# Kernel tuning notes

Measured on AMD Instinct MI355X. Metric: run time of the kernel, lower is better.

The kernel has to match this reference:

```python
import jax, jax.numpy as jnp
import numpy as np

N_NODES = 100000
N_EDGES = 600000
D = 128
EPS = 1e-12  # F.normalize default eps


def _l2_normalize(v, axis=1):
    n = jnp.linalg.norm(v, axis=axis, keepdims=True)
    return v / jnp.maximum(n, EPS)


def setup_inputs() -> dict:
    key = jax.random.key(0)
    k1, k2, k3, k4, k5 = jax.random.split(key, 5)
    x = jax.random.normal(k1, (N_NODES, D), dtype=jnp.float32)
    edge_index = jax.random.randint(k2, (2, N_EDGES), 0, N_NODES, dtype=jnp.int64)
    edge_weight = jax.random.uniform(k3, (N_EDGES,), dtype=jnp.float32)
    W = jax.random.normal(k4, (D, 2 * D), dtype=jnp.float32) / np.sqrt(2 * D)
    b = jax.random.normal(k5, (D,), dtype=jnp.float32) * 0.01
    return {"x": x, "edge_index": edge_index, "edge_weight": edge_weight, "W": W, "b": b}


def reference(x, edge_index, edge_weight, W, b):
    src, dst = edge_index[0], edge_index[1]
    # message: x_j * edge_weight; aggregate: scatter-add at destination nodes
    msgs = x[src] * edge_weight[:, None]                       # [E, D]
    grads = jax.ops.segment_sum(msgs, dst, num_segments=N_NODES)  # [N, D]
    norm_grads = _l2_normalize(grads, axis=1)
    out = jnp.concatenate((x, norm_grads), axis=1)             # [N, 2D]
    out = out @ W.T + b                                        # Linear(2D -> D)
    return _l2_normalize(out, axis=1)
```

## Files before the change

### kernel.cpp

```cpp
#include <hip/hip_runtime.h>
#include <stdint.h>

typedef __attribute__((ext_vector_type(8))) short short8;
typedef __attribute__((ext_vector_type(4))) float f32x4;

__device__ __forceinline__ uint32_t f2bf1(float f) {
  union { float f; uint32_t u; } c; c.f = f;
  return (c.u + 0x7FFFu + ((c.u >> 16) & 1u)) >> 16;
}
__device__ __forceinline__ uint32_t pack2bf(float lo, float hi) {
  return f2bf1(lo) | (f2bf1(hi) << 16);
}
__device__ __forceinline__ float bflo(uint32_t u) {
  union { uint32_t u; float f; } c; c.u = u << 16; return c.f;
}
__device__ __forceinline__ float bfhi(uint32_t u) {
  union { uint32_t u; float f; } c; c.u = u & 0xFFFF0000u; return c.f;
}

__global__ void __launch_bounds__(256) prep_kernel(
    const int* __restrict__ dst, uint32_t* __restrict__ deg,
    uint32_t* __restrict__ pos,
    const float* __restrict__ x, uint32_t* __restrict__ cat,
    const float* __restrict__ W, uint32_t* __restrict__ Wb,
    int E, int N, int cB, int xB) {
  int b = blockIdx.x;
  if (b < cB) {
    int e = b * 256 + threadIdx.x;
    if (e < E) pos[e] = atomicAdd(&deg[dst[e]], 1u);
  } else if (b < cB + xB) {
    int n = (b - cB) * 4 + (threadIdx.x >> 6);
    if (n >= N) return;
    int lane = threadIdx.x & 63;
    float2 xv = reinterpret_cast<const float2*>(x + (size_t)n * 128)[lane];
    cat[(size_t)n * 128 + lane] = pack2bf(xv.x, xv.y);
  } else {
    int i = (b - cB - xB) * 256 + threadIdx.x;
    if (i < 16384) {
      float2 wv = reinterpret_cast<const float2*>(W)[i];
      Wb[i] = pack2bf(wv.x, wv.y);
    }
  }
}

__global__ void __launch_bounds__(256) scan1_kernel(
    const uint32_t* __restrict__ deg, uint32_t* __restrict__ partial,
    uint32_t* __restrict__ bsum, int N) {
  __shared__ uint32_t sm[256];
  int t = threadIdx.x;
  int base = blockIdx.x * 1024 + t * 4;
  uint32_t d0 = 0, d1 = 0, d2 = 0, d3 = 0;
  if (base + 3 < N) {
    uint4 v = *reinterpret_cast<const uint4*>(deg + base);
    d0 = v.x; d1 = v.y; d2 = v.z; d3 = v.w;
  } else {
    if (base + 0 < N) d0 = deg[base + 0];
    if (base + 1 < N) d1 = deg[base + 1];
    if (base + 2 < N) d2 = deg[base + 2];
    if (base + 3 < N) d3 = deg[base + 3];
  }
  uint32_t s4 = d0 + d1 + d2 + d3;
  sm[t] = s4;
  uint32_t v = s4;
  __syncthreads();
  #pragma unroll
  for (int off = 1; off < 256; off <<= 1) {
    uint32_t u = (t >= off) ? sm[t - off] : 0u;
    __syncthreads();
    v += u;
    sm[t] = v;
    __syncthreads();
  }
  uint32_t ex = v - s4;
  if (base + 0 < N) partial[base + 0] = ex;
  if (base + 1 < N) partial[base + 1] = ex + d0;
  if (base + 2 < N) partial[base + 2] = ex + d0 + d1;
  if (base + 3 < N) partial[base + 3] = ex + d0 + d1 + d2;
  if (t == 255) bsum[blockIdx.x] = v;
}

__global__ void __launch_bounds__(1024) scan2_kernel(
    const uint32_t* __restrict__ bsum, uint32_t* __restrict__ boff, int nb) {
  __shared__ uint32_t sm[1024];
  int t = threadIdx.x;
  uint32_t s = (t < nb) ? bsum[t] : 0u;
  sm[t] = s;
  uint32_t v = s;
  __syncthreads();
  #pragma unroll
  for (int off = 1; off < 1024; off <<= 1) {
    uint32_t u = (t >= off) ? sm[t - off] : 0u;
    __syncthreads();
    v += u;
    sm[t] = v;
    __syncthreads();
  }
  if (t < nb) boff[t] = v - s;
}

__global__ void __launch_bounds__(256) fill_kernel(
    const int* __restrict__ src, const int* __restrict__ dst,
    const float* __restrict__ ew, const uint32_t* __restrict__ partial,
    const uint32_t* __restrict__ boff, const uint32_t* __restrict__ pos,
    uint2* __restrict__ pairs, int E) {
  int e = blockIdx.x * 256 + threadIdx.x;
  if (e < E) {
    int d = dst[e];
    union { float f; uint32_t u; } w; w.f = ew[e];
    pairs[partial[d] + boff[d >> 10] + pos[e]] = make_uint2((uint32_t)src[e], w.u);
  }
}

__global__ void __launch_bounds__(256) gather_kernel(
    const uint2* __restrict__ pairs, const uint32_t* __restrict__ partial,
    const uint32_t* __restrict__ boff, const uint32_t* __restrict__ deg,
    uint32_t* __restrict__ cat, int N) {
  int n = blockIdx.x * 4 + (threadIdx.x >> 6);
  if (n >= N) return;
  int lane = threadIdx.x & 63;
  int sg = lane >> 4;
  int sl = lane & 15;
  uint32_t base = partial[n] + boff[n >> 10];
  int dn = (int)deg[n];

  uint2 mp = (lane < dn) ? pairs[base + lane] : make_uint2(0u, 0u);

  float a[8] = {0.f, 0.f, 0.f, 0.f, 0.f, 0.f, 0.f, 0.f};
  int iters = (dn + 3) >> 2;
  for (int i = 0; i < iters; ++i) {
    int k = i * 4 + sg;
    uint32_t su = (uint32_t)__shfl((int)mp.x, k, 64);
    uint32_t wu = (uint32_t)__shfl((int)mp.y, k, 64);
    if (k < dn) {
      union { uint32_t u; float f; } w; w.u = wu;
      uint4 v = reinterpret_cast<const uint4*>(cat + (size_t)su * 128)[sl];
      a[0] += w.f * bflo(v.x); a[1] += w.f * bfhi(v.x);
      a[2] += w.f * bflo(v.y); a[3] += w.f * bfhi(v.y);
      a[4] += w.f * bflo(v.z); a[5] += w.f * bfhi(v.z);
      a[6] += w.f * bflo(v.w); a[7] += w.f * bfhi(v.w);
    }
  }
  for (int k = 64 + sg; k < dn; k += 4) {
    uint2 p = pairs[base + k];
    union { uint32_t u; float f; } w; w.u = p.y;
    uint4 v = reinterpret_cast<const uint4*>(cat + (size_t)p.x * 128)[sl];
    a[0] += w.f * bflo(v.x); a[1] += w.f * bfhi(v.x);
    a[2] += w.f * bflo(v.y); a[3] += w.f * bfhi(v.y);
    a[4] += w.f * bflo(v.z); a[5] += w.f * bfhi(v.z);
    a[6] += w.f * bflo(v.w); a[7] += w.f * bfhi(v.w);
  }

  #pragma unroll
  for (int j = 0; j < 8; ++j) {
    a[j] += __shfl_xor(a[j], 16, 64);
    a[j] += __shfl_xor(a[j], 32, 64);
  }
  float ss = 0.f;
  #pragma unroll
  for (int j = 0; j < 8; ++j) ss += a[j] * a[j];
  ss += __shfl_xor(ss, 1, 64);
  ss += __shfl_xor(ss, 2, 64);
  ss += __shfl_xor(ss, 4, 64);
  ss += __shfl_xor(ss, 8, 64);
  float scale = 1.0f / fmaxf(sqrtf(ss), 1e-12f);
  if (lane < 16) {
    uint4 o;
    o.x = pack2bf(a[0] * scale, a[1] * scale);
    o.y = pack2bf(a[2] * scale, a[3] * scale);
    o.z = pack2bf(a[4] * scale, a[5] * scale);
    o.w = pack2bf(a[6] * scale, a[7] * scale);
    reinterpret_cast<uint4*>(cat + (size_t)n * 128 + 64)[sl] = o;
  }
}

__global__ void __launch_bounds__(256) gemm_kernel(
    const ushort* __restrict__ cat, const ushort* __restrict__ Wb,
    const float* __restrict__ bias, float* __restrict__ out, int N) {
  int wid = threadIdx.x >> 6;
  int lane = threadIdx.x & 63;
  int node0 = (blockIdx.x * 4 + wid) * 32;
  if (node0 >= N) return;
  int r = lane & 15;
  int kg = lane >> 4;

  short8 a0[8], a1[8];
  const ushort* arow0 = cat + (size_t)(node0 + r) * 256 + kg * 8;
  const ushort* arow1 = arow0 + 16 * 256;
  #pragma unroll
  for (int ks = 0; ks < 8; ++ks) {
    a0[ks] = *reinterpret_cast<const short8*>(arow0 + ks * 32);
    a1[ks] = *reinterpret_cast<const short8*>(arow1 + ks * 32);
  }

  f32x4 acc0[8], acc1[8];
  #pragma unroll
  for (int nt = 0; nt < 8; ++nt) {
    acc0[nt] = (f32x4){0.f, 0.f, 0.f, 0.f};
    acc1[nt] = (f32x4){0.f, 0.f, 0.f, 0.f};
  }

  const ushort* wbase = Wb + kg * 8;
  #pragma unroll
  for (int nt = 0; nt < 8; ++nt) {
    const ushort* wrow = wbase + (size_t)(nt * 16 + r) * 256;
    #pragma unroll
    for (int ks = 0; ks < 8; ++ks) {
      short8 bfrag = *reinterpret_cast<const short8*>(wrow + ks * 32);
      acc0[nt] = __builtin_amdgcn_mfma_f32_16x16x32_bf16(a0[ks], bfrag, acc0[nt], 0, 0, 0);
      acc1[nt] = __builtin_amdgcn_mfma_f32_16x16x32_bf16(a1[ks], bfrag, acc1[nt], 0, 0, 0);
    }
  }

  float bv[8];
  #pragma unroll
  for (int nt = 0; nt < 8; ++nt) bv[nt] = bias[nt * 16 + r];

  #pragma unroll
  for (int st = 0; st < 2; ++st) {
    f32x4* acc = st ? acc1 : acc0;
    int nodeb = node0 + st * 16;
    #pragma unroll
    for (int reg = 0; reg < 4; ++reg) {
      float ss = 0.f;
      #pragma unroll
      for (int nt = 0; nt < 8; ++nt) {
        float v = acc[nt][reg] + bv[nt];
        acc[nt][reg] = v;
        ss += v * v;
      }
      ss += __shfl_xor(ss, 1, 64);
      ss += __shfl_xor(ss, 2, 64);
      ss += __shfl_xor(ss, 4, 64);
      ss += __shfl_xor(ss, 8, 64);
      float scale = 1.0f / fmaxf(sqrtf(ss), 1e-12f);
      float* orow = out + (size_t)(nodeb + kg * 4 + reg) * 128;
      #pragma unroll
      for (int nt = 0; nt < 8; ++nt)
        orow[nt * 16 + r] = acc[nt][reg] * scale;
    }
  }
}

extern "C" void kernel_launch(void* const* d_in, const int* in_sizes, int n_in,
                              void* d_out, int out_size, void* d_ws, size_t ws_size,
                              hipStream_t stream) {
  const float* x    = (const float*)d_in[0];
  const int*   ei   = (const int*)d_in[1];
  const float* ew   = (const float*)d_in[2];
  const float* W    = (const float*)d_in[3];
  const float* bias = (const float*)d_in[4];
  float* out = (float*)d_out;

  int N = in_sizes[0] / 128;
  int E = in_sizes[1] / 2;
  const int* src = ei;
  const int* dst = ei + E;
  int nb = (N + 1023) / 1024;

  uint32_t* cat = (uint32_t*)d_ws;
  uint32_t* Wb  = cat + (size_t)N * 128;

  uint32_t* o       = (uint32_t*)d_out;
  uint32_t* deg     = o;
  uint32_t* partial = o + N;
  uint32_t* bsum    = o + 2 * (size_t)N;
  uint32_t* boff    = o + 2 * (size_t)N + 1024;
  uint2*    pairs   = (uint2*)(o + 2 * (size_t)N + 2048);
  uint32_t* pos     = o + 2 * (size_t)N + 2048 + 2 * (size_t)E;

  int cB = (E + 255) / 256;
  int xB = (N + 3) / 4;
  hipMemsetAsync(deg, 0, (size_t)N * sizeof(uint32_t), stream);
  prep_kernel<<<cB + xB + 64, 256, 0, stream>>>(dst, deg, pos, x, cat, W, Wb,
                                                E, N, cB, xB);
  scan1_kernel<<<nb, 256, 0, stream>>>(deg, partial, bsum, N);
  scan2_kernel<<<1, 1024, 0, stream>>>(bsum, boff, nb);
  fill_kernel<<<(E + 255) / 256, 256, 0, stream>>>(src, dst, ew, partial, boff,
                                                   pos, pairs, E);
  gather_kernel<<<(N + 3) / 4, 256, 0, stream>>>(pairs, partial, boff, deg, cat, N);
  int ntiles32 = (N + 31) / 32;
  gemm_kernel<<<(ntiles32 + 3) / 4, 256, 0, stream>>>(
      (const ushort*)cat, (const ushort*)Wb, bias, out, N);
}
```

Measured before the change: 147.3 us.

## Restructure GEMM as persistent blocks with register-resident W slices and prefetch

```diff
diff --git a/kernel.cpp b/kernel.cpp
--- a/kernel.cpp
+++ b/kernel.cpp
@@ -173,71 +173,80 @@
   }
 }
 
-__global__ void __launch_bounds__(256) gemm_kernel(
+__global__ void __launch_bounds__(512) gemm_kernel(
     const ushort* __restrict__ cat, const ushort* __restrict__ Wb,
     const float* __restrict__ bias, float* __restrict__ out, int N) {
-  int wid = threadIdx.x >> 6;
-  int lane = threadIdx.x & 63;
-  int node0 = (blockIdx.x * 4 + wid) * 32;
-  if (node0 >= N) return;
-  int r = lane & 15;
+  __shared__ float sP[2][8][16];
+  int t = threadIdx.x;
+  int wid = t >> 6;
+  int lane = t & 63;
+  int c = lane & 15;
   int kg = lane >> 4;
 
-  short8 a0[8], a1[8];
-  const ushort* arow0 = cat + (size_t)(node0 + r) * 256 + kg * 8;
-  const ushort* arow1 = arow0 + 16 * 256;
-  #pragma unroll
-  for (int ks = 0; ks < 8; ++ks) {
-    a0[ks] = *reinterpret_cast<const short8*>(arow0 + ks * 32);
-    a1[ks] = *reinterpret_cast<const short8*>(arow1 + ks * 32);
-  }
-
-  f32x4 acc0[8], acc1[8];
-  #pragma unroll
-  for (int nt = 0; nt < 8; ++nt) {
-    acc0[nt] = (f32x4){0.f, 0.f, 0.f, 0.f};
-    acc1[nt] = (f32x4){0.f, 0.f, 0.f, 0.f};
-  }
-
-  const ushort* wbase = Wb + kg * 8;
-  #pragma unroll
-  for (int nt = 0; nt < 8; ++nt) {
-    const ushort* wrow = wbase + (size_t)(nt * 16 + r) * 256;
-    #pragma unroll
-    for (int ks = 0; ks < 8; ++ks) {
-      short8 bfrag = *reinterpret_cast<const short8*>(wrow + ks * 32);
-      acc0[nt] = __builtin_amdgcn_mfma_f32_16x16x32_bf16(a0[ks], bfrag, acc0[nt], 0, 0, 0);
-      acc1[nt] = __builtin_amdgcn_mfma_f32_16x16x32_bf16(a1[ks], bfrag, acc1[nt], 0, 0, 0);
-    }
-  }
-
-  float bv[8];
-  #pragma unroll
-  for (int nt = 0; nt < 8; ++nt) bv[nt] = bias[nt * 16 + r];
-
-  #pragma unroll
-  for (int st = 0; st < 2; ++st) {
-    f32x4* acc = st ? acc1 : acc0;
-    int nodeb = node0 + st * 16;
+  short8 b[8];
+  {
+    const ushort* wrow = Wb + (size_t)(wid * 16 + c) * 256 + kg * 8;
+    #pragma unroll
+    for (int ks = 0; ks < 8; ++ks)
+      b[ks] = *reinterpret_cast<const short8*>(wrow + ks * 32);
+  }
+  float bv = bias[wid * 16 + c];
+
+  int ntiles = (N + 15) >> 4;
+  int par = 0;
+  int tile = blockIdx.x;
+  short8 a[8];
+  if (tile < ntiles) {
+    int rw = min(tile * 16 + c, N - 1);
+    const ushort* arow = cat + (size_t)rw * 256 + kg * 8;
+    #pragma unroll
+    for (int ks = 0; ks < 8; ++ks)
+      a[ks] = *reinterpret_cast<const short8*>(arow + ks * 32);
+  }
+
+  for (; tile < ntiles; tile += gridDim.x) {
+    short8 an[8];
+    int tn = tile + gridDim.x;
+    if (tn < ntiles) {
+      int rw = min(tn * 16 + c, N - 1);
+      const ushort* arow = cat + (size_t)rw * 256 + kg * 8;
+      #pragma unroll
+      for (int ks = 0; ks < 8; ++ks)
+        an[ks] = *reinterpret_cast<const short8*>(arow + ks * 32);
+    }
+
+    f32x4 acc = (f32x4){0.f, 0.f, 0.f, 0.f};
+    #pragma unroll
+    for (int ks = 0; ks < 8; ++ks)
+      acc = __builtin_amdgcn_mfma_f32_16x16x32_bf16(a[ks], b[ks], acc, 0, 0, 0);
+
     #pragma unroll
     for (int reg = 0; reg < 4; ++reg) {
-      float ss = 0.f;
+      float v = acc[reg] + bv;
+      acc[reg] = v;
+      float ssp = v * v;
+      ssp += __shfl_xor(ssp, 1, 64);
+      ssp += __shfl_xor(ssp, 2, 64);
+      ssp += __shfl_xor(ssp, 4, 64);
+      ssp += __shfl_xor(ssp, 8, 64);
+      if (c == 0) sP[par][wid][kg * 4 + reg] = ssp;
+    }
+    __syncthreads();
+
+    int node0 = tile * 16;
+    #pragma unroll
+    for (int reg = 0; reg < 4; ++reg) {
+      int row = kg * 4 + reg;
+      float tot = 0.f;
       #pragma unroll
-      for (int nt = 0; nt < 8; ++nt) {
-        float v = acc[nt][reg] + bv[nt];
-        acc[nt][reg] = v;
-        ss += v * v;
-      }
-      ss += __shfl_xor(ss, 1, 64);
-      ss += __shfl_xor(ss, 2, 64);
-      ss += __shfl_xor(ss, 4, 64);
-      ss += __shfl_xor(ss, 8, 64);
-      float scale = 1.0f / fmaxf(sqrtf(ss), 1e-12f);
-      float* orow = out + (size_t)(nodeb + kg * 4 + reg) * 128;
-      #pragma unroll
-      for (int nt = 0; nt < 8; ++nt)
-        orow[nt * 16 + r] = acc[nt][reg] * scale;
-    }
+      for (int w = 0; w < 8; ++w) tot += sP[par][w][row];
+      float scale = 1.0f / fmaxf(sqrtf(tot), 1e-12f);
+      if (node0 + row < N)
+        out[(size_t)(node0 + row) * 128 + wid * 16 + c] = acc[reg] * scale;
+    }
+    par ^= 1;
+    #pragma unroll
+    for (int ks = 0; ks < 8; ++ks) a[ks] = an[ks];
   }
 }
 
@@ -278,7 +287,8 @@
   fill_kernel<<<(E + 255) / 256, 256, 0, stream>>>(src, dst, ew, partial, boff,
                                                    pos, pairs, E);
   gather_kernel<<<(N + 3) / 4, 256, 0, stream>>>(pairs, partial, boff, deg, cat, N);
-  int ntiles32 = (N + 31) / 32;
-  gemm_kernel<<<(ntiles32 + 3) / 4, 256, 0, stream>>>(
+  int ntiles16 = (N + 15) / 16;
+  int g = ntiles16 < 1024 ? ntiles16 : 1024;
+  gemm_kernel<<<g, 512, 0, stream>>>(
       (const ushort*)cat, (const ushort*)Wb, bias, out, N);
 }
```

Measured after the change: 166.8 us. 13.3% more time.

## Store GEMM operands in MFMA fragment order and keep dense bf16 x for gather

Applied to the files above, without the earlier changes.

```diff
diff --git a/kernel.cpp b/kernel.cpp
--- a/kernel.cpp
+++ b/kernel.cpp
@@ -18,27 +18,49 @@
   union { uint32_t u; float f; } c; c.u = u & 0xFFFF0000u; return c.f;
 }
 
+
 __global__ void __launch_bounds__(256) prep_kernel(
     const int* __restrict__ dst, uint32_t* __restrict__ deg,
     uint32_t* __restrict__ pos,
-    const float* __restrict__ x, uint32_t* __restrict__ cat,
-    const float* __restrict__ W, uint32_t* __restrict__ Wb,
-    int E, int N, int cB, int xB) {
+    const float* __restrict__ x, uint32_t* __restrict__ xbf,
+    uint32_t* __restrict__ catf,
+    const float* __restrict__ W, uint32_t* __restrict__ wf,
+    int E, int N, int cB, int xB, int fB) {
   int b = blockIdx.x;
+  int ti = threadIdx.x;
   if (b < cB) {
-    int e = b * 256 + threadIdx.x;
+    int e = b * 256 + ti;
     if (e < E) pos[e] = atomicAdd(&deg[dst[e]], 1u);
   } else if (b < cB + xB) {
-    int n = (b - cB) * 4 + (threadIdx.x >> 6);
+    int n = (b - cB) * 4 + (ti >> 6);
     if (n >= N) return;
-    int lane = threadIdx.x & 63;
+    int lane = ti & 63;
     float2 xv = reinterpret_cast<const float2*>(x + (size_t)n * 128)[lane];
-    cat[(size_t)n * 128 + lane] = pack2bf(xv.x, xv.y);
+    xbf[(size_t)n * 64 + lane] = pack2bf(xv.x, xv.y);
+  } else if (b < cB + xB + fB) {
+    int t = b - cB - xB;
+    int ks = ti >> 6;
+    int lane = ti & 63;
+    int node = t * 16 + (lane & 15);
+    const float* xp = x + (size_t)node * 128 + ks * 32 + (lane >> 4) * 8;
+    float4 f0 = reinterpret_cast<const float4*>(xp)[0];
+    float4 f1 = reinterpret_cast<const float4*>(xp)[1];
+    uint4 pk;
+    pk.x = pack2bf(f0.x, f0.y); pk.y = pack2bf(f0.z, f0.w);
+    pk.z = pack2bf(f1.x, f1.y); pk.w = pack2bf(f1.z, f1.w);
+    reinterpret_cast<uint4*>(catf)[(size_t)(t * 8 + ks) * 64 + lane] = pk;
   } else {
-    int i = (b - cB - xB) * 256 + threadIdx.x;
-    if (i < 16384) {
-      float2 wv = reinterpret_cast<const float2*>(W)[i];
-      Wb[i] = pack2bf(wv.x, wv.y);
+    int ch = (b - cB - xB - fB) * 256 + ti;
+    if (ch < 4096) {
+      int nt = ch >> 9, ks = (ch >> 6) & 7, lane = ch & 63;
+      int row = nt * 16 + (lane & 15);
+      const float* wp = W + (size_t)row * 256 + ks * 32 + (lane >> 4) * 8;
+      float4 f0 = reinterpret_cast<const float4*>(wp)[0];
+      float4 f1 = reinterpret_cast<const float4*>(wp)[1];
+      uint4 pk;
+      pk.x = pack2bf(f0.x, f0.y); pk.y = pack2bf(f0.z, f0.w);
+      pk.z = pack2bf(f1.x, f1.y); pk.w = pack2bf(f1.z, f1.w);
+      reinterpret_cast<uint4*>(wf)[ch] = pk;
     }
   }
 }
@@ -114,7 +136,7 @@
 __global__ void __launch_bounds__(256) gather_kernel(
     const uint2* __restrict__ pairs, const uint32_t* __restrict__ partial,
     const uint32_t* __restrict__ boff, const uint32_t* __restrict__ deg,
-    uint32_t* __restrict__ cat, int N) {
+    const uint32_t* __restrict__ xbf, uint32_t* __restrict__ catf, int N) {
   int n = blockIdx.x * 4 + (threadIdx.x >> 6);
   if (n >= N) return;
   int lane = threadIdx.x & 63;
@@ -133,7 +155,7 @@
     uint32_t wu = (uint32_t)__shfl((int)mp.y, k, 64);
     if (k < dn) {
       union { uint32_t u; float f; } w; w.u = wu;
-      uint4 v = reinterpret_cast<const uint4*>(cat + (size_t)su * 128)[sl];
+      uint4 v = reinterpret_cast<const uint4*>(xbf + (size_t)su * 64)[sl];
       a[0] += w.f * bflo(v.x); a[1] += w.f * bfhi(v.x);
       a[2] += w.f * bflo(v.y); a[3] += w.f * bfhi(v.y);
       a[4] += w.f * bflo(v.z); a[5] += w.f * bfhi(v.z);
@@ -143,7 +165,7 @@
   for (int k = 64 + sg; k < dn; k += 4) {
     uint2 p = pairs[base + k];
     union { uint32_t u; float f; } w; w.u = p.y;
-    uint4 v = reinterpret_cast<const uint4*>(cat + (size_t)p.x * 128)[sl];
+    uint4 v = reinterpret_cast<const uint4*>(xbf + (size_t)p.x * 64)[sl];
     a[0] += w.f * bflo(v.x); a[1] += w.f * bfhi(v.x);
     a[2] += w.f * bflo(v.y); a[3] += w.f * bfhi(v.y);
     a[4] += w.f * bflo(v.z); a[5] += w.f * bfhi(v.z);
@@ -169,27 +191,31 @@
     o.y = pack2bf(a[2] * scale, a[3] * scale);
     o.z = pack2bf(a[4] * scale, a[5] * scale);
     o.w = pack2bf(a[6] * scale, a[7] * scale);
-    reinterpret_cast<uint4*>(cat + (size_t)n * 128 + 64)[sl] = o;
+    int t = n >> 4, rr = n & 15;
+    reinterpret_cast<uint4*>(catf)[
+        (size_t)(t * 8 + 4 + (sl >> 2)) * 64 + (sl & 3) * 16 + rr] = o;
   }
 }
 
 __global__ void __launch_bounds__(256) gemm_kernel(
-    const ushort* __restrict__ cat, const ushort* __restrict__ Wb,
+    const uint32_t* __restrict__ catf, const uint32_t* __restrict__ wf,
     const float* __restrict__ bias, float* __restrict__ out, int N) {
   int wid = threadIdx.x >> 6;
   int lane = threadIdx.x & 63;
-  int node0 = (blockIdx.x * 4 + wid) * 32;
+  int tile = blockIdx.x * 4 + wid;
+  int node0 = tile * 32;
   if (node0 >= N) return;
   int r = lane & 15;
   int kg = lane >> 4;
+  int t0 = tile * 2;
 
   short8 a0[8], a1[8];
-  const ushort* arow0 = cat + (size_t)(node0 + r) * 256 + kg * 8;
-  const ushort* arow1 = arow0 + 16 * 256;
   #pragma unroll
   for (int ks = 0; ks < 8; ++ks) {
-    a0[ks] = *reinterpret_cast<const short8*>(arow0 + ks * 32);
-    a1[ks] = *reinterpret_cast<const short8*>(arow1 + ks * 32);
+    a0[ks] = *reinterpret_cast<const short8*>(
+        catf + ((size_t)(t0 * 8 + ks) * 64 + lane) * 4);
+    a1[ks] = *reinterpret_cast<const short8*>(
+        catf + ((size_t)((t0 + 1) * 8 + ks) * 64 + lane) * 4);
   }
 
   f32x4 acc0[8], acc1[8];
@@ -199,13 +225,12 @@
     acc1[nt] = (f32x4){0.f, 0.f, 0.f, 0.f};
   }
 
-  const ushort* wbase = Wb + kg * 8;
   #pragma unroll
   for (int nt = 0; nt < 8; ++nt) {
-    const ushort* wrow = wbase + (size_t)(nt * 16 + r) * 256;
     #pragma unroll
     for (int ks = 0; ks < 8; ++ks) {
-      short8 bfrag = *reinterpret_cast<const short8*>(wrow + ks * 32);
+      short8 bfrag = *reinterpret_cast<const short8*>(
+          wf + ((size_t)(nt * 8 + ks) * 64 + lane) * 4);
       acc0[nt] = __builtin_amdgcn_mfma_f32_16x16x32_bf16(a0[ks], bfrag, acc0[nt], 0, 0, 0);
       acc1[nt] = __builtin_amdgcn_mfma_f32_16x16x32_bf16(a1[ks], bfrag, acc1[nt], 0, 0, 0);
     }
@@ -257,8 +282,8 @@
   const int* dst = ei + E;
   int nb = (N + 1023) / 1024;
 
-  uint32_t* cat = (uint32_t*)d_ws;
-  uint32_t* Wb  = cat + (size_t)N * 128;
+  uint32_t* catf = (uint32_t*)d_ws;
+  uint32_t* wf   = catf + (size_t)N * 128;
 
   uint32_t* o       = (uint32_t*)d_out;
   uint32_t* deg     = o;
@@ -267,18 +292,20 @@
   uint32_t* boff    = o + 2 * (size_t)N + 1024;
   uint2*    pairs   = (uint2*)(o + 2 * (size_t)N + 2048);
   uint32_t* pos     = o + 2 * (size_t)N + 2048 + 2 * (size_t)E;
+  uint32_t* xbf     = o + 2 * (size_t)N + 2048 + 3 * (size_t)E;
 
   int cB = (E + 255) / 256;
   int xB = (N + 3) / 4;
+  int fB = (N + 15) / 16;
   hipMemsetAsync(deg, 0, (size_t)N * sizeof(uint32_t), stream);
-  prep_kernel<<<cB + xB + 64, 256, 0, stream>>>(dst, deg, pos, x, cat, W, Wb,
-                                                E, N, cB, xB);
+  prep_kernel<<<cB + xB + fB + 16, 256, 0, stream>>>(
+      dst, deg, pos, x, xbf, catf, W, wf, E, N, cB, xB, fB);
   scan1_kernel<<<nb, 256, 0, stream>>>(deg, partial, bsum, N);
   scan2_kernel<<<1, 1024, 0, stream>>>(bsum, boff, nb);
   fill_kernel<<<(E + 255) / 256, 256, 0, stream>>>(src, dst, ew, partial, boff,
                                                    pos, pairs, E);
-  gather_kernel<<<(N + 3) / 4, 256, 0, stream>>>(pairs, partial, boff, deg, cat, N);
+  gather_kernel<<<(N + 3) / 4, 256, 0, stream>>>(pairs, partial, boff, deg,
+                                                 xbf, catf, N);
   int ntiles32 = (N + 31) / 32;
-  gemm_kernel<<<(ntiles32 + 3) / 4, 256, 0, stream>>>(
-      (const ushort*)cat, (const ushort*)Wb, bias, out, N);
-}
+  gemm_kernel<<<(ntiles32 + 3) / 4, 256, 0, stream>>>(catf, wf, bias, out, N);
+}
```

Result: no change. 146.7 us (-0.4%).
